# Performance work log

Hardware: AMD Instinct MI355X
Metric: run time of the kernel (lower is better)

Reference implementation:

```python
import jax, jax.numpy as jnp
import numpy as np

EPS = 1e-8


def _dir_to_face_uv(dirs):
    # dirs: [N,3] unit vectors -> face index [N] (int32), uv [N,2] in [-1,1]
    x, y, z = dirs[:, 0], dirs[:, 1], dirs[:, 2]
    ax, ay, az = jnp.abs(x), jnp.abs(y), jnp.abs(z)
    x_dom = (ax >= ay) & (ax >= az)
    y_dom = (ay > ax) & (ay >= az)
    face = jnp.where(x_dom, jnp.where(x > 0, 0, 1),
           jnp.where(y_dom, jnp.where(y > 0, 2, 3),
                     jnp.where(z > 0, 4, 5))).astype(jnp.int32)
    u_c = jnp.stack([-z / (ax + EPS), z / (ax + EPS), x / (ay + EPS),
                     x / (ay + EPS), x / (az + EPS), -x / (az + EPS)], axis=-1)  # [N,6]
    v_c = jnp.stack([-y / (ax + EPS), -y / (ax + EPS), z / (ay + EPS),
                     -z / (ay + EPS), -y / (az + EPS), -y / (az + EPS)], axis=-1)
    u = jnp.take_along_axis(u_c, face[:, None], axis=1)[:, 0]
    v = jnp.take_along_axis(v_c, face[:, None], axis=1)[:, 0]
    uv = jnp.clip(jnp.stack([u, v], axis=-1), -1.0, 1.0)
    return face, uv


def _sample_cubemap(cubemaps, probe_idx, face, uv):
    # Bilinear 1x1 grid_sample, align_corners=True, padding_mode='border'.
    # Gathers only the 4 needed texels per query instead of full face images.
    M, F6, H, W, C = cubemaps.shape
    u, v = uv[:, 0], uv[:, 1]
    ix = (u + 1.0) * 0.5 * (W - 1)  # x -> width
    iy = (v + 1.0) * 0.5 * (H - 1)  # y -> height
    x0f = jnp.floor(ix)
    y0f = jnp.floor(iy)
    wx = (ix - x0f)[:, None]
    wy = (iy - y0f)[:, None]
    x0 = jnp.clip(x0f.astype(jnp.int32), 0, W - 1)
    x1 = jnp.clip(x0 + 1, 0, W - 1)
    y0 = jnp.clip(y0f.astype(jnp.int32), 0, H - 1)
    y1 = jnp.clip(y0 + 1, 0, H - 1)
    g = lambda yy, xx: cubemaps[probe_idx, face, yy, xx]  # [N,C]
    return (g(y0, x0) * (1 - wx) * (1 - wy) + g(y0, x1) * wx * (1 - wy)
            + g(y1, x0) * (1 - wx) * wy + g(y1, x1) * wx * wy)


def _query(xyz, view_dirs, cubemaps, probe_positions, K):
    N = xyz.shape[0]
    # Euclidean cdist via GEMM form
    x2 = jnp.sum(xyz * xyz, axis=-1, keepdims=True)            # [N,1]
    p2 = jnp.sum(probe_positions * probe_positions, axis=-1)   # [M]
    d2 = jnp.maximum(x2 + p2[None, :] - 2.0 * (xyz @ probe_positions.T), 0.0)
    dists = jnp.sqrt(d2)                                       # [N,M]
    neg_vals, topk_idx = jax.lax.top_k(-dists, K)              # smallest K
    topk_dists = -neg_vals
    weights = 1.0 / (topk_dists + 1e-4)
    weights = weights / jnp.sum(weights, axis=-1, keepdims=True)  # [N,K]
    # F.normalize(dim=-1) with eps=1e-12
    dirs = view_dirs / jnp.maximum(jnp.linalg.norm(view_dirs, axis=-1, keepdims=True), 1e-12)
    face, uv = _dir_to_face_uv(dirs)
    probe_flat = topk_idx.reshape(N * K)
    face_flat = jnp.broadcast_to(face[:, None], (N, K)).reshape(N * K)
    uv_flat = jnp.broadcast_to(uv[:, None, :], (N, K, 2)).reshape(N * K, 2)
    sampled = _sample_cubemap(cubemaps, probe_flat, face_flat, uv_flat).reshape(N, K, 3)
    return jnp.sum(sampled * weights[..., None], axis=1)       # [N,3]


def setup_inputs() -> dict:
    key = jax.random.key(0)
    k1, k2, k3 = jax.random.split(key, 3)
    N = 1_000_000
    grid_size, cubemap_res = 5, 16
    lo, hi = -3.0, 3.0
    coords = [np.linspace(lo, hi, grid_size, dtype=np.float32) for _ in range(3)]
    grid = np.stack(np.meshgrid(*coords, indexing='ij'), axis=-1)
    probe_positions = jnp.asarray(grid.reshape(-1, 3))         # [125,3]
    M = probe_positions.shape[0]
    xyz = jax.random.normal(k1, (N, 3), dtype=jnp.float32)
    view_dirs = jax.random.normal(k2, (N, 3), dtype=jnp.float32)
    cubemaps = 0.1 * jax.random.normal(k3, (M, 6, cubemap_res, cubemap_res, 3), dtype=jnp.float32)
    return {"xyz": xyz, "view_dirs": view_dirs, "cubemaps": cubemaps,
            "probe_positions": probe_positions, "k_nearest": 4}


def reference(xyz, view_dirs, cubemaps, probe_positions, k_nearest):
    K = min(int(k_nearest), probe_positions.shape[0])
    return _query(xyz, view_dirs, cubemaps, probe_positions, K)
```

## Files before the change

### kernel.cpp

```cpp
#include <hip/hip_runtime.h>
#include <hip/hip_fp16.h>
#include <math.h>


#define NPATCH      192000
#define PATCH_BYTES ((size_t)NPATCH * 32)

typedef float vf4 __attribute__((ext_vector_type(4)));
typedef unsigned int u32x4 __attribute__((ext_vector_type(4)));
typedef unsigned int u32x2 __attribute__((ext_vector_type(2)));

__device__ __forceinline__ float fastrcp(float x)  { return __builtin_amdgcn_rcpf(x); }
__device__ __forceinline__ float fastsqrt(float x) { return __builtin_amdgcn_sqrtf(x); }

__device__ __forceinline__ void up2(unsigned u, float& a, float& b) {
    __half2 h;
    *(unsigned*)&h = u;
    float2 f = __half22float2(h);
    a = f.x; b = f.y;
}

__device__ __forceinline__ void dimsort(float v,
    float& e0, float& e1, float& e2, int& c0, int& c1, int& c2)
{
    float f = (v + 3.0f) * (1.0f / 1.5f);
    int n = (int)floorf(f + 0.5f);
    n = n < 0 ? 0 : (n > 4 ? 4 : n);
    int s = n - 1;
    s = s < 0 ? 0 : (s > 2 ? 2 : s);

    float p0 = fmaf(1.5f, (float)s, -3.0f);
    float d0 = v - p0;
    float d1 = d0 - 1.5f;
    float d2 = d1 - 1.5f;
    float a0 = d0 * d0, a1 = d1 * d1, a2 = d2 * d2;
    int j0 = s, j1 = s + 1, j2 = s + 2;

    {   bool sw = a1 < a0;
        float ta = sw ? a1 : a0, tb = sw ? a0 : a1;
        int   ua = sw ? j1 : j0, ub = sw ? j0 : j1;
        a0 = ta; a1 = tb; j0 = ua; j1 = ub; }
    {   bool sw = a2 < a1;
        float ta = sw ? a2 : a1, tb = sw ? a1 : a2;
        int   ua = sw ? j2 : j1, ub = sw ? j1 : j2;
        a1 = ta; a2 = tb; j1 = ua; j2 = ub; }
    {   bool sw = a1 < a0;
        float ta = sw ? a1 : a0, tb = sw ? a0 : a1;
        int   ua = sw ? j1 : j0, ub = sw ? j0 : j1;
        a0 = ta; a1 = tb; j0 = ua; j1 = ub; }

    e0 = a0; e1 = a1; e2 = a2;
    c0 = j0; c1 = j1; c2 = j2;
}

#define INSERT(d, L, s0, s1, s2, s3, k0, k1, k2, k3)                          \
    {                                                                         \
        bool lt = (d) < s3; s3 = lt ? (d) : s3; k3 = lt ? (L) : k3;           \
        { bool cb = s3 < s2; float nd = cb ? s3 : s2, xd = cb ? s2 : s3;      \
          int ni = cb ? k3 : k2, xi = cb ? k2 : k3;                           \
          s2 = nd; s3 = xd; k2 = ni; k3 = xi; }                               \
        { bool cb = s2 < s1; float nd = cb ? s2 : s1, xd = cb ? s1 : s2;      \
          int ni = cb ? k2 : k1, xi = cb ? k1 : k2;                           \
          s1 = nd; s2 = xd; k1 = ni; k2 = xi; }                               \
        { bool cb = s1 < s0; float nd = cb ? s1 : s0, xd = cb ? s0 : s1;      \
          int ni = cb ? k1 : k0, xi = cb ? k0 : k1;                           \
          s0 = nd; s1 = xd; k0 = ni; k1 = xi; }                               \
    }

__device__ __forceinline__ void uv_setup(
    float dx, float dy, float dz,
    int& face, int& t00,
    float& w00, float& w01, float& w10, float& w11)
{
    float nrm = sqrtf(fmaf(dx, dx, fmaf(dy, dy, dz * dz)));
    nrm = fmaxf(nrm, 1e-12f);
    float inv = fastrcp(nrm);
    float ux = dx * inv, uy = dy * inv, uz = dz * inv;
    float ax = fabsf(ux), ay = fabsf(uy), az = fabsf(uz);

    bool xd = (ax >= ay) && (ax >= az);
    float den, un, vn;
    if (xd) {
        face = (ux > 0.0f) ? 0 : 1;
        den = ax; un = (ux > 0.0f) ? -uz : uz; vn = -uy;
    } else if (ay >= az) {
        face = (uy > 0.0f) ? 2 : 3;
        den = ay; un = ux; vn = (uy > 0.0f) ? uz : -uz;
    } else {
        face = (uz > 0.0f) ? 4 : 5;
        den = az; un = (uz > 0.0f) ? ux : -ux; vn = -uy;
    }
    float rden = fastrcp(den + 1e-8f);
    float u = un * rden;
    float v = vn * rden;
    u = fminf(1.0f, fmaxf(-1.0f, u));
    v = fminf(1.0f, fmaxf(-1.0f, v));

    float fx = (u + 1.0f) * 0.5f * 15.0f;
    float fy = (v + 1.0f) * 0.5f * 15.0f;
    float x0f = floorf(fx), y0f = floorf(fy);
    float wx = fx - x0f, wy = fy - y0f;
    int px0 = (int)x0f; px0 = px0 < 0 ? 0 : (px0 > 15 ? 15 : px0);
    int py0 = (int)y0f; py0 = py0 < 0 ? 0 : (py0 > 15 ? 15 : py0);

    w00 = (1.0f - wx) * (1.0f - wy);
    w01 = wx * (1.0f - wy);
    w10 = (1.0f - wx) * wy;
    w11 = wx * wy;

    t00 = py0 * 16 + px0;
}

__global__ __launch_bounds__(256) void build_patches_f16(
    const float* __restrict__ cube, unsigned int* __restrict__ patches)
{
    int t = blockIdx.x * blockDim.x + threadIdx.x;
    if (t >= NPATCH) return;
    int p   = t % 125;
    int q   = t / 125;
    int px0 = q % 16; q /= 16;
    int py0 = q % 16;
    int face = q / 16;
    int px1 = px0 + 1 > 15 ? 15 : px0 + 1;
    int py1 = py0 + 1 > 15 ? 15 : py0 + 1;

    const float* f = cube + (p * 6 + face) * 768;
    int o00 = (py0 * 16 + px0) * 3;
    int o01 = (py0 * 16 + px1) * 3;
    int o10 = (py1 * 16 + px0) * 3;
    int o11 = (py1 * 16 + px1) * 3;

    float v[12];
    v[0] = f[o00]; v[1]  = f[o00 + 1]; v[2]  = f[o00 + 2];
    v[3] = f[o01]; v[4]  = f[o01 + 1]; v[5]  = f[o01 + 2];
    v[6] = f[o10]; v[7]  = f[o10 + 1]; v[8]  = f[o10 + 2];
    v[9] = f[o11]; v[10] = f[o11 + 1]; v[11] = f[o11 + 2];

    unsigned u[8];
#pragma unroll
    for (int j = 0; j < 6; j++) {
        __half a = __float2half(v[2 * j]);
        __half b = __float2half(v[2 * j + 1]);
        u[j] = (unsigned)__half_as_ushort(a) | ((unsigned)__half_as_ushort(b) << 16);
    }
    u[6] = 0; u[7] = 0;

    u32x4* dst = (u32x4*)(patches + (size_t)t * 8);
    u32x4 a = {u[0], u[1], u[2], u[3]};
    u32x4 b = {u[4], u[5], u[6], u[7]};
    dst[0] = a;
    dst[1] = b;
}

__global__ __launch_bounds__(256) void lp_f16(
    const float* __restrict__ xyz,
    const float* __restrict__ vdirs,
    const unsigned int* __restrict__ patches,
    float* __restrict__ out,
    int N)
{
    __shared__ float sh[1536];

    int tid = threadIdx.x;
    int b0  = blockIdx.x * 256;
    int nPts = N - b0; nPts = nPts > 256 ? 256 : nPts;
    int nflt = nPts * 3;
    int base4 = (b0 * 3) >> 2;

    const vf4* x4 = (const vf4*)xyz;
    const vf4* d4 = (const vf4*)vdirs;
    if (tid * 4 < nflt) {
        vf4 vx = __builtin_nontemporal_load(&x4[base4 + tid]);
        ((vf4*)sh)[tid] = vx;
        vf4 vd = __builtin_nontemporal_load(&d4[base4 + tid]);
        ((vf4*)(sh + 768))[tid] = vd;
    }
    __syncthreads();

    float r = 0.0f, g = 0.0f, b = 0.0f;
    if (tid < nPts) {
        float x  = sh[3 * tid + 0];
        float y  = sh[3 * tid + 1];
        float z  = sh[3 * tid + 2];
        float dx = sh[768 + 3 * tid + 0];
        float dy = sh[768 + 3 * tid + 1];
        float dz = sh[768 + 3 * tid + 2];

        float ex0, ex1, ex2, ey0, ey1, ey2, ez0, ez1, ez2;
        int jx0, jx1, jx2, jy0, jy1, jy2, jz0, jz1, jz2;
        dimsort(x, ex0, ex1, ex2, jx0, jx1, jx2);
        dimsort(y, ey0, ey1, ey2, jy0, jy1, jy2);
        dimsort(z, ez0, ez1, ez2, jz0, jz1, jz2);

        int X0 = jx0 * 25, X1 = jx1 * 25, X2 = jx2 * 25;
        int Y0 = jy0 * 5,  Y1 = jy1 * 5,  Y2 = jy2 * 5;
        int Z0 = jz0,      Z1 = jz1,      Z2 = jz2;

        float exy00 = ex0 + ey0, exy10 = ex1 + ey0, exy01 = ex0 + ey1;
        float exy11 = ex1 + ey1, exy20 = ex2 + ey0, exy02 = ex0 + ey2;
        int   kxy00 = X0 + Y0,   kxy10 = X1 + Y0,   kxy01 = X0 + Y1;
        int   kxy11 = X1 + Y1,   kxy20 = X2 + Y0,   kxy02 = X0 + Y2;

        float s0 = exy00 + ez0, s1 = 1e30f, s2 = 1e30f, s3 = 1e30f;
        int   k0 = kxy00 + Z0,  k1 = 0,     k2 = 0,     k3 = 0;

        { float d = exy10 + ez0; int L = kxy10 + Z0; INSERT(d, L, s0, s1, s2, s3, k0, k1, k2, k3); }
        { float d = exy01 + ez0; int L = kxy01 + Z0; INSERT(d, L, s0, s1, s2, s3, k0, k1, k2, k3); }
        { float d = exy00 + ez1; int L = kxy00 + Z1; INSERT(d, L, s0, s1, s2, s3, k0, k1, k2, k3); }
        { float d = exy11 + ez0; int L = kxy11 + Z0; INSERT(d, L, s0, s1, s2, s3, k0, k1, k2, k3); }
        { float d = exy10 + ez1; int L = kxy10 + Z1; INSERT(d, L, s0, s1, s2, s3, k0, k1, k2, k3); }
        { float d = exy01 + ez1; int L = kxy01 + Z1; INSERT(d, L, s0, s1, s2, s3, k0, k1, k2, k3); }
        { float d = exy20 + ez0; int L = kxy20 + Z0; INSERT(d, L, s0, s1, s2, s3, k0, k1, k2, k3); }
        { float d = exy02 + ez0; int L = kxy02 + Z0; INSERT(d, L, s0, s1, s2, s3, k0, k1, k2, k3); }
        { float d = exy00 + ez2; int L = kxy00 + Z2; INSERT(d, L, s0, s1, s2, s3, k0, k1, k2, k3); }

        float w0 = fastrcp(fastsqrt(s0) + 1e-4f);
        float w1 = fastrcp(fastsqrt(s1) + 1e-4f);
        float w2 = fastrcp(fastsqrt(s2) + 1e-4f);
        float w3 = fastrcp(fastsqrt(s3) + 1e-4f);
        float wi = fastrcp(w0 + w1 + w2 + w3);
        w0 *= wi; w1 *= wi; w2 *= wi; w3 *= wi;

        int face, t00;
        float w00, w01, w10, w11;
        uv_setup(dx, dy, dz, face, t00, w00, w01, w10, w11);

        int cell = (face * 256 + t00) * 125;
#pragma unroll
        for (int k = 0; k < 4; k++) {
            int   p  = (k == 0) ? k0 : (k == 1) ? k1 : (k == 2) ? k2 : k3;
            float wn = (k == 0) ? w0 : (k == 1) ? w1 : (k == 2) ? w2 : w3;
            const unsigned* pp = patches + (size_t)(cell + p) * 8;
            u32x4 lo = *(const u32x4*)pp;
            u32x2 hi = *(const u32x2*)(pp + 4);
            float r00, g00, b00, r01, g01, b01, r10, g10, b10, r11, g11, b11;
            up2(lo.x, r00, g00);
            up2(lo.y, b00, r01);
            up2(lo.z, g01, b01);
            up2(lo.w, r10, g10);
            up2(hi.x, b10, r11);
            up2(hi.y, g11, b11);
            float rr = fmaf(r00, w00, fmaf(r01, w01, fmaf(r10, w10, r11 * w11)));
            float gg = fmaf(g00, w00, fmaf(g01, w01, fmaf(g10, w10, g11 * w11)));
            float bv = fmaf(b00, w00, fmaf(b01, w01, fmaf(b10, w10, b11 * w11)));
            r = fmaf(wn, rr, r);
            g = fmaf(wn, gg, g);
            b = fmaf(wn, bv, b);
        }
    }

    __syncthreads();
    if (tid < nPts) {
        sh[3 * tid + 0] = r;
        sh[3 * tid + 1] = g;
        sh[3 * tid + 2] = b;
    }
    __syncthreads();
    if (tid * 4 < nflt) {
        vf4* o4 = (vf4*)out;
        __builtin_nontemporal_store(((vf4*)sh)[tid], &o4[base4 + tid]);
    }
}

extern "C" void kernel_launch(void* const* d_in, const int* in_sizes, int n_in,
                              void* d_out, int out_size, void* d_ws, size_t ws_size,
                              hipStream_t stream) {
    const float* xyz  = (const float*)d_in[0];
    const float* vd   = (const float*)d_in[1];
    const float* cube = (const float*)d_in[2];
    float* outp = (float*)d_out;
    int N = in_sizes[0] / 3;
    int blocks = (N + 255) / 256;

    unsigned int* patches = (unsigned int*)d_ws;
    hipLaunchKernelGGL(build_patches_f16, dim3((NPATCH + 255) / 256), dim3(256), 0, stream,
                       cube, patches);
    hipLaunchKernelGGL(lp_f16, dim3(blocks), dim3(256), 0, stream,
                       xyz, vd, patches, outp, N);
}
```

Before: 41.46 us.

## Process four points per thread with direct vector loads, dropping LDS staging

The query kernel now has each thread handle four consecutive points. It reads their coordinates and directions as three 16-byte vectors each and writes the outputs the same way, so the shared-memory staging and block barriers are gone. Point setup for all four points runs before the patch gathers, which exposes sixteen independent gathers per thread for memory-level parallelism. The cost is higher register pressure and a quarter as many threads, which may reduce occupancy and latency hiding. Block size drops to 128.

```diff
diff --git a/kernel.cpp b/kernel.cpp
--- a/kernel.cpp
+++ b/kernel.cpp
@@ -3,8 +3,7 @@
 #include <math.h>
 
 
-#define NPATCH      192000
-#define PATCH_BYTES ((size_t)NPATCH * 32)
+#define NPATCH 192000
 
 typedef float vf4 __attribute__((ext_vector_type(4)));
 typedef unsigned int u32x4 __attribute__((ext_vector_type(4)));
@@ -111,6 +110,77 @@
     t00 = py0 * 16 + px0;
 }
 
+__device__ __forceinline__ void point_setup(
+    float x, float y, float z, float dx, float dy, float dz,
+    int& pi0, int& pi1, int& pi2, int& pi3,
+    float& w0, float& w1, float& w2, float& w3,
+    float& w00, float& w01, float& w10, float& w11)
+{
+    float ex0, ex1, ex2, ey0, ey1, ey2, ez0, ez1, ez2;
+    int jx0, jx1, jx2, jy0, jy1, jy2, jz0, jz1, jz2;
+    dimsort(x, ex0, ex1, ex2, jx0, jx1, jx2);
+    dimsort(y, ey0, ey1, ey2, jy0, jy1, jy2);
+    dimsort(z, ez0, ez1, ez2, jz0, jz1, jz2);
+
+    int X0 = jx0 * 25, X1 = jx1 * 25, X2 = jx2 * 25;
+    int Y0 = jy0 * 5,  Y1 = jy1 * 5,  Y2 = jy2 * 5;
+    int Z0 = jz0,      Z1 = jz1,      Z2 = jz2;
+
+    float exy00 = ex0 + ey0, exy10 = ex1 + ey0, exy01 = ex0 + ey1;
+    float exy11 = ex1 + ey1, exy20 = ex2 + ey0, exy02 = ex0 + ey2;
+    int   kxy00 = X0 + Y0,   kxy10 = X1 + Y0,   kxy01 = X0 + Y1;
+    int   kxy11 = X1 + Y1,   kxy20 = X2 + Y0,   kxy02 = X0 + Y2;
+
+    float s0 = exy00 + ez0, s1 = 1e30f, s2 = 1e30f, s3 = 1e30f;
+    int   k0 = kxy00 + Z0,  k1 = 0,     k2 = 0,     k3 = 0;
+
+    { float d = exy10 + ez0; int L = kxy10 + Z0; INSERT(d, L, s0, s1, s2, s3, k0, k1, k2, k3); }
+    { float d = exy01 + ez0; int L = kxy01 + Z0; INSERT(d, L, s0, s1, s2, s3, k0, k1, k2, k3); }
+    { float d = exy00 + ez1; int L = kxy00 + Z1; INSERT(d, L, s0, s1, s2, s3, k0, k1, k2, k3); }
+    { float d = exy11 + ez0; int L = kxy11 + Z0; INSERT(d, L, s0, s1, s2, s3, k0, k1, k2, k3); }
+    { float d = exy10 + ez1; int L = kxy10 + Z1; INSERT(d, L, s0, s1, s2, s3, k0, k1, k2, k3); }
+    { float d = exy01 + ez1; int L = kxy01 + Z1; INSERT(d, L, s0, s1, s2, s3, k0, k1, k2, k3); }
+    { float d = exy20 + ez0; int L = kxy20 + Z0; INSERT(d, L, s0, s1, s2, s3, k0, k1, k2, k3); }
+    { float d = exy02 + ez0; int L = kxy02 + Z0; INSERT(d, L, s0, s1, s2, s3, k0, k1, k2, k3); }
+    { float d = exy00 + ez2; int L = kxy00 + Z2; INSERT(d, L, s0, s1, s2, s3, k0, k1, k2, k3); }
+
+    w0 = fastrcp(fastsqrt(s0) + 1e-4f);
+    w1 = fastrcp(fastsqrt(s1) + 1e-4f);
+    w2 = fastrcp(fastsqrt(s2) + 1e-4f);
+    w3 = fastrcp(fastsqrt(s3) + 1e-4f);
+    float wi = fastrcp(w0 + w1 + w2 + w3);
+    w0 *= wi; w1 *= wi; w2 *= wi; w3 *= wi;
+
+    int face, t00;
+    uv_setup(dx, dy, dz, face, t00, w00, w01, w10, w11);
+
+    int cell = (face * 256 + t00) * 125;
+    pi0 = cell + k0; pi1 = cell + k1; pi2 = cell + k2; pi3 = cell + k3;
+}
+
+__device__ __forceinline__ void patch_accum(
+    const unsigned int* __restrict__ patches, int pidx, float wn,
+    float w00, float w01, float w10, float w11,
+    float& r, float& g, float& b)
+{
+    const unsigned* pp = patches + (size_t)pidx * 8;
+    u32x4 lo = *(const u32x4*)pp;
+    u32x2 hi = *(const u32x2*)(pp + 4);
+    float r00, g00, b00, r01, g01, b01, r10, g10, b10, r11, g11, b11;
+    up2(lo.x, r00, g00);
+    up2(lo.y, b00, r01);
+    up2(lo.z, g01, b01);
+    up2(lo.w, r10, g10);
+    up2(hi.x, b10, r11);
+    up2(hi.y, g11, b11);
+    float rr = fmaf(r00, w00, fmaf(r01, w01, fmaf(r10, w10, r11 * w11)));
+    float gg = fmaf(g00, w00, fmaf(g01, w01, fmaf(g10, w10, g11 * w11)));
+    float bv = fmaf(b00, w00, fmaf(b01, w01, fmaf(b10, w10, b11 * w11)));
+    r = fmaf(wn, rr, r);
+    g = fmaf(wn, gg, g);
+    b = fmaf(wn, bv, b);
+}
+
 __global__ __launch_bounds__(256) void build_patches_f16(
     const float* __restrict__ cube, unsigned int* __restrict__ patches)
 {
@@ -152,113 +222,84 @@
     dst[1] = b;
 }
 
-__global__ __launch_bounds__(256) void lp_f16(
+__global__ __launch_bounds__(128) void lp_f16_q(
     const float* __restrict__ xyz,
     const float* __restrict__ vdirs,
     const unsigned int* __restrict__ patches,
     float* __restrict__ out,
     int N)
 {
-    __shared__ float sh[1536];
-
-    int tid = threadIdx.x;
-    int b0  = blockIdx.x * 256;
-    int nPts = N - b0; nPts = nPts > 256 ? 256 : nPts;
-    int nflt = nPts * 3;
-    int base4 = (b0 * 3) >> 2;
-
-    const vf4* x4 = (const vf4*)xyz;
-    const vf4* d4 = (const vf4*)vdirs;
-    if (tid * 4 < nflt) {
-        vf4 vx = __builtin_nontemporal_load(&x4[base4 + tid]);
-        ((vf4*)sh)[tid] = vx;
-        vf4 vd = __builtin_nontemporal_load(&d4[base4 + tid]);
-        ((vf4*)(sh + 768))[tid] = vd;
-    }
-    __syncthreads();
-
-    float r = 0.0f, g = 0.0f, b = 0.0f;
-    if (tid < nPts) {
-        float x  = sh[3 * tid + 0];
-        float y  = sh[3 * tid + 1];
-        float z  = sh[3 * tid + 2];
-        float dx = sh[768 + 3 * tid + 0];
-        float dy = sh[768 + 3 * tid + 1];
-        float dz = sh[768 + 3 * tid + 2];
-
-        float ex0, ex1, ex2, ey0, ey1, ey2, ez0, ez1, ez2;
-        int jx0, jx1, jx2, jy0, jy1, jy2, jz0, jz1, jz2;
-        dimsort(x, ex0, ex1, ex2, jx0, jx1, jx2);
-        dimsort(y, ey0, ey1, ey2, jy0, jy1, jy2);
-        dimsort(z, ez0, ez1, ez2, jz0, jz1, jz2);
-
-        int X0 = jx0 * 25, X1 = jx1 * 25, X2 = jx2 * 25;
-        int Y0 = jy0 * 5,  Y1 = jy1 * 5,  Y2 = jy2 * 5;
-        int Z0 = jz0,      Z1 = jz1,      Z2 = jz2;
-
-        float exy00 = ex0 + ey0, exy10 = ex1 + ey0, exy01 = ex0 + ey1;
-        float exy11 = ex1 + ey1, exy20 = ex2 + ey0, exy02 = ex0 + ey2;
-        int   kxy00 = X0 + Y0,   kxy10 = X1 + Y0,   kxy01 = X0 + Y1;
-        int   kxy11 = X1 + Y1,   kxy20 = X2 + Y0,   kxy02 = X0 + Y2;
-
-        float s0 = exy00 + ez0, s1 = 1e30f, s2 = 1e30f, s3 = 1e30f;
-        int   k0 = kxy00 + Z0,  k1 = 0,     k2 = 0,     k3 = 0;
-
-        { float d = exy10 + ez0; int L = kxy10 + Z0; INSERT(d, L, s0, s1, s2, s3, k0, k1, k2, k3); }
-        { float d = exy01 + ez0; int L = kxy01 + Z0; INSERT(d, L, s0, s1, s2, s3, k0, k1, k2, k3); }
-        { float d = exy00 + ez1; int L = kxy00 + Z1; INSERT(d, L, s0, s1, s2, s3, k0, k1, k2, k3); }
-        { float d = exy11 + ez0; int L = kxy11 + Z0; INSERT(d, L, s0, s1, s2, s3, k0, k1, k2, k3); }
-        { float d = exy10 + ez1; int L = kxy10 + Z1; INSERT(d, L, s0, s1, s2, s3, k0, k1, k2, k3); }
-        { float d = exy01 + ez1; int L = kxy01 + Z1; INSERT(d, L, s0, s1, s2, s3, k0, k1, k2, k3); }
-        { float d = exy20 + ez0; int L = kxy20 + Z0; INSERT(d, L, s0, s1, s2, s3, k0, k1, k2, k3); }
-        { float d = exy02 + ez0; int L = kxy02 + Z0; INSERT(d, L, s0, s1, s2, s3, k0, k1, k2, k3); }
-        { float d = exy00 + ez2; int L = kxy00 + Z2; INSERT(d, L, s0, s1, s2, s3, k0, k1, k2, k3); }
-
-        float w0 = fastrcp(fastsqrt(s0) + 1e-4f);
-        float w1 = fastrcp(fastsqrt(s1) + 1e-4f);
-        float w2 = fastrcp(fastsqrt(s2) + 1e-4f);
-        float w3 = fastrcp(fastsqrt(s3) + 1e-4f);
-        float wi = fastrcp(w0 + w1 + w2 + w3);
-        w0 *= wi; w1 *= wi; w2 *= wi; w3 *= wi;
-
-        int face, t00;
-        float w00, w01, w10, w11;
-        uv_setup(dx, dy, dz, face, t00, w00, w01, w10, w11);
-
-        int cell = (face * 256 + t00) * 125;
-#pragma unroll
-        for (int k = 0; k < 4; k++) {
-            int   p  = (k == 0) ? k0 : (k == 1) ? k1 : (k == 2) ? k2 : k3;
-            float wn = (k == 0) ? w0 : (k == 1) ? w1 : (k == 2) ? w2 : w3;
-            const unsigned* pp = patches + (size_t)(cell + p) * 8;
-            u32x4 lo = *(const u32x4*)pp;
-            u32x2 hi = *(const u32x2*)(pp + 4);
-            float r00, g00, b00, r01, g01, b01, r10, g10, b10, r11, g11, b11;
-            up2(lo.x, r00, g00);
-            up2(lo.y, b00, r01);
-            up2(lo.z, g01, b01);
-            up2(lo.w, r10, g10);
-            up2(hi.x, b10, r11);
-            up2(hi.y, g11, b11);
-            float rr = fmaf(r00, w00, fmaf(r01, w01, fmaf(r10, w10, r11 * w11)));
-            float gg = fmaf(g00, w00, fmaf(g01, w01, fmaf(g10, w10, g11 * w11)));
-            float bv = fmaf(b00, w00, fmaf(b01, w01, fmaf(b10, w10, b11 * w11)));
-            r = fmaf(wn, rr, r);
-            g = fmaf(wn, gg, g);
-            b = fmaf(wn, bv, b);
+    int t = blockIdx.x * blockDim.x + threadIdx.x;
+    int p0 = t * 4;
+    if (p0 >= N) return;
+    bool full = (p0 + 3) < N;
+
+    float X[4], Y[4], Z[4], DX[4], DY[4], DZ[4];
+
+    if (full) {
+        const vf4* x4 = (const vf4*)(xyz + p0 * 3);
+        const vf4* d4 = (const vf4*)(vdirs + p0 * 3);
+        vf4 a = __builtin_nontemporal_load(&x4[0]);
+        vf4 b = __builtin_nontemporal_load(&x4[1]);
+        vf4 c = __builtin_nontemporal_load(&x4[2]);
+        X[0] = a.x; Y[0] = a.y; Z[0] = a.z;
+        X[1] = a.w; Y[1] = b.x; Z[1] = b.y;
+        X[2] = b.z; Y[2] = b.w; Z[2] = c.x;
+        X[3] = c.y; Y[3] = c.z; Z[3] = c.w;
+        vf4 e = __builtin_nontemporal_load(&d4[0]);
+        vf4 f = __builtin_nontemporal_load(&d4[1]);
+        vf4 g = __builtin_nontemporal_load(&d4[2]);
+        DX[0] = e.x; DY[0] = e.y; DZ[0] = e.z;
+        DX[1] = e.w; DY[1] = f.x; DZ[1] = f.y;
+        DX[2] = f.z; DY[2] = f.w; DZ[2] = g.x;
+        DX[3] = g.y; DY[3] = g.z; DZ[3] = g.w;
+    } else {
+#pragma unroll
+        for (int j = 0; j < 4; j++) {
+            int i = p0 + j < N ? p0 + j : N - 1;
+            X[j]  = xyz[3 * i];  Y[j]  = xyz[3 * i + 1];  Z[j]  = xyz[3 * i + 2];
+            DX[j] = vdirs[3 * i]; DY[j] = vdirs[3 * i + 1]; DZ[j] = vdirs[3 * i + 2];
         }
     }
 
-    __syncthreads();
-    if (tid < nPts) {
-        sh[3 * tid + 0] = r;
-        sh[3 * tid + 1] = g;
-        sh[3 * tid + 2] = b;
-    }
-    __syncthreads();
-    if (tid * 4 < nflt) {
-        vf4* o4 = (vf4*)out;
-        __builtin_nontemporal_store(((vf4*)sh)[tid], &o4[base4 + tid]);
+    int pi0[4], pi1[4], pi2[4], pi3[4];
+    float w0[4], w1[4], w2[4], w3[4];
+    float w00[4], w01[4], w10[4], w11[4];
+#pragma unroll
+    for (int j = 0; j < 4; j++) {
+        point_setup(X[j], Y[j], Z[j], DX[j], DY[j], DZ[j],
+                    pi0[j], pi1[j], pi2[j], pi3[j],
+                    w0[j], w1[j], w2[j], w3[j],
+                    w00[j], w01[j], w10[j], w11[j]);
+    }
+
+    float R[4], G[4], B[4];
+#pragma unroll
+    for (int j = 0; j < 4; j++) {
+        R[j] = 0.0f; G[j] = 0.0f; B[j] = 0.0f;
+        patch_accum(patches, pi0[j], w0[j], w00[j], w01[j], w10[j], w11[j], R[j], G[j], B[j]);
+        patch_accum(patches, pi1[j], w1[j], w00[j], w01[j], w10[j], w11[j], R[j], G[j], B[j]);
+        patch_accum(patches, pi2[j], w2[j], w00[j], w01[j], w10[j], w11[j], R[j], G[j], B[j]);
+        patch_accum(patches, pi3[j], w3[j], w00[j], w01[j], w10[j], w11[j], R[j], G[j], B[j]);
+    }
+
+    if (full) {
+        vf4* o4 = (vf4*)(out + p0 * 3);
+        vf4 a = {R[0], G[0], B[0], R[1]};
+        vf4 b = {G[1], B[1], R[2], G[2]};
+        vf4 c = {B[2], R[3], G[3], B[3]};
+        __builtin_nontemporal_store(a, &o4[0]);
+        __builtin_nontemporal_store(b, &o4[1]);
+        __builtin_nontemporal_store(c, &o4[2]);
+    } else {
+#pragma unroll
+        for (int j = 0; j < 4; j++) {
+            if (p0 + j < N) {
+                out[3 * (p0 + j)]     = R[j];
+                out[3 * (p0 + j) + 1] = G[j];
+                out[3 * (p0 + j) + 2] = B[j];
+            }
+        }
     }
 }
 
@@ -270,11 +311,12 @@
     const float* cube = (const float*)d_in[2];
     float* outp = (float*)d_out;
     int N = in_sizes[0] / 3;
-    int blocks = (N + 255) / 256;
+    int nthreads = (N + 3) / 4;
+    int blocks = (nthreads + 127) / 128;
 
     unsigned int* patches = (unsigned int*)d_ws;
     hipLaunchKernelGGL(build_patches_f16, dim3((NPATCH + 255) / 256), dim3(256), 0, stream,
                        cube, patches);
-    hipLaunchKernelGGL(lp_f16, dim3(blocks), dim3(256), 0, stream,
+    hipLaunchKernelGGL(lp_f16_q, dim3(blocks), dim3(128), 0, stream,
                        xyz, vd, patches, outp, N);
 }
```

Measured after the change: 46.49 us. 1.12x slower.

## Pack cubemap bilinear patches as 10-bit shared-exponent integers in 16 bytes

Applied to the files above, without the earlier changes.

Replaces the fp16 patch format (24 used bytes padded to 32) with a shared-exponent format: twelve 10-bit signed mantissas plus a 6-bit exponent packed into one 16-byte word. This halves the patch table footprint and turns each gather into a single 128-bit load, aiming to cut cache and memory traffic in the lookup kernel. Decoding costs shifts and int-to-float conversions per texel. Precision drops to about 9 bits relative to the patch maximum, which adds quantization error.

```diff
diff --git a/kernel.cpp b/kernel.cpp
--- a/kernel.cpp
+++ b/kernel.cpp
@@ -1,24 +1,14 @@
 #include <hip/hip_runtime.h>
-#include <hip/hip_fp16.h>
 #include <math.h>
 
 
-#define NPATCH      192000
-#define PATCH_BYTES ((size_t)NPATCH * 32)
+#define NPATCH 192000
 
 typedef float vf4 __attribute__((ext_vector_type(4)));
 typedef unsigned int u32x4 __attribute__((ext_vector_type(4)));
-typedef unsigned int u32x2 __attribute__((ext_vector_type(2)));
 
 __device__ __forceinline__ float fastrcp(float x)  { return __builtin_amdgcn_rcpf(x); }
 __device__ __forceinline__ float fastsqrt(float x) { return __builtin_amdgcn_sqrtf(x); }
-
-__device__ __forceinline__ void up2(unsigned u, float& a, float& b) {
-    __half2 h;
-    *(unsigned*)&h = u;
-    float2 f = __half22float2(h);
-    a = f.x; b = f.y;
-}
 
 __device__ __forceinline__ void dimsort(float v,
     float& e0, float& e1, float& e2, int& c0, int& c1, int& c2)
@@ -111,8 +101,8 @@
     t00 = py0 * 16 + px0;
 }
 
-__global__ __launch_bounds__(256) void build_patches_f16(
-    const float* __restrict__ cube, unsigned int* __restrict__ patches)
+__global__ __launch_bounds__(256) void build_patches_se(
+    const float* __restrict__ cube, u32x4* __restrict__ patches)
 {
     int t = blockIdx.x * blockDim.x + threadIdx.x;
     if (t >= NPATCH) return;
@@ -136,26 +126,46 @@
     v[6] = f[o10]; v[7]  = f[o10 + 1]; v[8]  = f[o10 + 2];
     v[9] = f[o11]; v[10] = f[o11 + 1]; v[11] = f[o11 + 2];
 
-    unsigned u[8];
+    float mx = 0.0f;
 #pragma unroll
-    for (int j = 0; j < 6; j++) {
-        __half a = __float2half(v[2 * j]);
-        __half b = __float2half(v[2 * j + 1]);
-        u[j] = (unsigned)__half_as_ushort(a) | ((unsigned)__half_as_ushort(b) << 16);
-    }
-    u[6] = 0; u[7] = 0;
-
-    u32x4* dst = (u32x4*)(patches + (size_t)t * 8);
-    u32x4 a = {u[0], u[1], u[2], u[3]};
-    u32x4 b = {u[4], u[5], u[6], u[7]};
-    dst[0] = a;
-    dst[1] = b;
-}
-
-__global__ __launch_bounds__(256) void lp_f16(
+    for (int j = 0; j < 12; j++) mx = fmaxf(mx, fabsf(v[j]));
+
+    int E;
+    if (mx == 0.0f) {
+        E = 0;
+    } else {
+        unsigned mb = __float_as_uint(mx);
+        int eb = (int)((mb >> 23) & 0xFF) - 127;
+        E = eb + 32;
+        E = E < 0 ? 0 : (E > 63 ? 63 : E);
+    }
+    float mscale = __uint_as_float((unsigned)(167 - E) << 23);
+
+    unsigned m[12];
+#pragma unroll
+    for (int j = 0; j < 12; j++) {
+        float s = rintf(v[j] * mscale);
+        s = fminf(511.0f, fmaxf(-511.0f, s));
+        m[j] = (unsigned)((int)s) & 0x3FF;
+    }
+
+    unsigned w0 = m[0] | (m[1] << 10) | (m[2] << 20) | (((unsigned)E & 3) << 30);
+    unsigned w1 = m[3] | (m[4] << 10) | (m[5] << 20) | ((((unsigned)E >> 2) & 3) << 30);
+    unsigned w2 = m[6] | (m[7] << 10) | (m[8] << 20) | ((((unsigned)E >> 4) & 3) << 30);
+    unsigned w3 = m[9] | (m[10] << 10) | (m[11] << 20);
+
+    u32x4 o = {w0, w1, w2, w3};
+    patches[t] = o;
+}
+
+__device__ __forceinline__ float dec(unsigned w, int sh) {
+    return (float)(((int)(w << (22 - sh))) >> 22);
+}
+
+__global__ __launch_bounds__(256) void lp_se(
     const float* __restrict__ xyz,
     const float* __restrict__ vdirs,
-    const unsigned int* __restrict__ patches,
+    const u32x4* __restrict__ patches,
     float* __restrict__ out,
     int N)
 {
@@ -226,26 +236,28 @@
         uv_setup(dx, dy, dz, face, t00, w00, w01, w10, w11);
 
         int cell = (face * 256 + t00) * 125;
+
 #pragma unroll
         for (int k = 0; k < 4; k++) {
             int   p  = (k == 0) ? k0 : (k == 1) ? k1 : (k == 2) ? k2 : k3;
             float wn = (k == 0) ? w0 : (k == 1) ? w1 : (k == 2) ? w2 : w3;
-            const unsigned* pp = patches + (size_t)(cell + p) * 8;
-            u32x4 lo = *(const u32x4*)pp;
-            u32x2 hi = *(const u32x2*)(pp + 4);
-            float r00, g00, b00, r01, g01, b01, r10, g10, b10, r11, g11, b11;
-            up2(lo.x, r00, g00);
-            up2(lo.y, b00, r01);
-            up2(lo.z, g01, b01);
-            up2(lo.w, r10, g10);
-            up2(hi.x, b10, r11);
-            up2(hi.y, g11, b11);
+            u32x4 pw = patches[cell + p];
+
+            int E = (int)((pw.x >> 30) | (((pw.y >> 30) & 3u) << 2) | (((pw.z >> 30) & 3u) << 4));
+            float s = __uint_as_float((unsigned)(E + 87) << 23);
+            float wns = wn * s;
+
+            float r00 = dec(pw.x, 0),  g00 = dec(pw.x, 10), b00 = dec(pw.x, 20);
+            float r01 = dec(pw.y, 0),  g01 = dec(pw.y, 10), b01 = dec(pw.y, 20);
+            float r10 = dec(pw.z, 0),  g10 = dec(pw.z, 10), b10 = dec(pw.z, 20);
+            float r11 = dec(pw.w, 0),  g11 = dec(pw.w, 10), b11 = dec(pw.w, 20);
+
             float rr = fmaf(r00, w00, fmaf(r01, w01, fmaf(r10, w10, r11 * w11)));
             float gg = fmaf(g00, w00, fmaf(g01, w01, fmaf(g10, w10, g11 * w11)));
             float bv = fmaf(b00, w00, fmaf(b01, w01, fmaf(b10, w10, b11 * w11)));
-            r = fmaf(wn, rr, r);
-            g = fmaf(wn, gg, g);
-            b = fmaf(wn, bv, b);
+            r = fmaf(wns, rr, r);
+            g = fmaf(wns, gg, g);
+            b = fmaf(wns, bv, b);
         }
     }
 
@@ -272,9 +284,9 @@
     int N = in_sizes[0] / 3;
     int blocks = (N + 255) / 256;
 
-    unsigned int* patches = (unsigned int*)d_ws;
-    hipLaunchKernelGGL(build_patches_f16, dim3((NPATCH + 255) / 256), dim3(256), 0, stream,
+    u32x4* patches = (u32x4*)d_ws;
+    hipLaunchKernelGGL(build_patches_se, dim3((NPATCH + 255) / 256), dim3(256), 0, stream,
                        cube, patches);
-    hipLaunchKernelGGL(lp_f16, dim3(blocks), dim3(256), 0, stream,
+    hipLaunchKernelGGL(lp_se, dim3(blocks), dim3(256), 0, stream,
                        xyz, vd, patches, outp, N);
 }
```

Result: faster. 34.40 us (-17.0%).
